# Kernel optimization log

Measured on AMD Instinct MI355X. Metric: run time of the kernel, lower is better.

Reference implementation:

```python
import jax, jax.numpy as jnp
import numpy as np

B, S, HID = 2, 2048, 2048
NH, NKV = 32, 8
HD = HID // NH          # 64
G = NH // NKV           # 4 query heads per kv head
ROPE_BASE = 10000.0


def _rope_cos_sin(seq_len, head_dim, dtype):
    inv_freq = 1.0 / (ROPE_BASE ** (jnp.arange(0, head_dim, 2, dtype=jnp.float32) / head_dim))
    freqs = jnp.arange(seq_len, dtype=jnp.float32)[:, None] * inv_freq[None, :]  # [S, HD/2]
    cos = jnp.cos(freqs)
    sin = jnp.sin(freqs)
    # torch code does cos.repeat(1, 2): tile along last dim -> [S, HD]
    cos = jnp.concatenate([cos, cos], axis=-1).astype(dtype)
    sin = jnp.concatenate([sin, sin], axis=-1).astype(dtype)
    return cos, sin


def _rotate_half(x):
    x1, x2 = jnp.split(x, 2, axis=-1)
    return jnp.concatenate([-x2, x1], axis=-1)


def setup_inputs() -> dict:
    key = jax.random.key(0)
    ks = jax.random.split(key, 5)
    sc = 0.02
    return {
        "hidden_states": jax.random.normal(ks[0], (B, S, HID), dtype=jnp.float32),
        "wq": jax.random.normal(ks[1], (HID, HID), dtype=jnp.float32) * sc,
        "wk": jax.random.normal(ks[2], (NKV * HD, HID), dtype=jnp.float32) * sc,
        "wv": jax.random.normal(ks[3], (NKV * HD, HID), dtype=jnp.float32) * sc,
        "wo": jax.random.normal(ks[4], (HID, HID), dtype=jnp.float32) * sc,
    }


def reference(hidden_states, wq, wk, wv, wo):
    b, s, _ = hidden_states.shape
    # projections (torch Linear: y = x @ W^T)
    q = (hidden_states @ wq.T).reshape(b, s, NH, HD).transpose(0, 2, 1, 3)   # [B,NH,S,HD]
    k = (hidden_states @ wk.T).reshape(b, s, NKV, HD).transpose(0, 2, 1, 3)  # [B,NKV,S,HD]
    v = (hidden_states @ wv.T).reshape(b, s, NKV, HD).transpose(0, 2, 1, 3)  # [B,NKV,S,HD]

    cos, sin = _rope_cos_sin(s, HD, q.dtype)  # [S,HD]
    q = q * cos + _rotate_half(q) * sin
    k = k * cos + _rotate_half(k) * sin

    # GQA: group query heads per kv head instead of repeat_interleave (same math)
    qg = q.reshape(b, NKV, G, s, HD)
    scale = HD ** -0.5
    scores = jnp.einsum('bkgsd,bktd->bkgst', qg, k) * scale     # [B,NKV,G,S,S]
    attn = jax.nn.softmax(scores, axis=-1)
    out = jnp.einsum('bkgst,bktd->bkgsd', attn, v)              # [B,NKV,G,S,HD]
    out = out.reshape(b, NH, s, HD).transpose(0, 2, 1, 3).reshape(b, s, HID)
    return out @ wo.T
```

## Files before the change

### kernel.cpp

```cpp
#include <hip/hip_runtime.h>
#include <stdint.h>

typedef __attribute__((ext_vector_type(8))) short bf16x8;
typedef __attribute__((ext_vector_type(4))) short bf16x4;
typedef __attribute__((ext_vector_type(4))) float f32x4;
typedef __attribute__((ext_vector_type(4))) unsigned u32x4;
typedef __attribute__((ext_vector_type(2))) unsigned u32x2;

#define S_LEN 2048
#define HIDDEN 2048
#define N_HEADS 32
#define N_KV 8
#define HEAD_DIM 64
#define KVD (N_KV * HEAD_DIM)

__device__ __forceinline__ float bf2f(short u) {
  return __builtin_bit_cast(float, ((unsigned)(unsigned short)u) << 16);
}
__device__ __forceinline__ short f2bf(float f) {
  unsigned u = __builtin_bit_cast(unsigned, f);
  u += 0x7FFFu + ((u >> 16) & 1u);
  return (short)(u >> 16);
}
__device__ __forceinline__ unsigned cvtpk(float lo, float hi) {
  unsigned r;
  asm("v_cvt_pk_bf16_f32 %0, %1, %2" : "=v"(r) : "v"(lo), "v"(hi));
  return r;
}
__device__ __forceinline__ bf16x8 cvt8(f32x4 lo, f32x4 hi) {
  bf16x8 r;
#pragma unroll
  for (int j = 0; j < 4; ++j) { r[j] = f2bf(lo[j]); r[j + 4] = f2bf(hi[j]); }
  return r;
}
__device__ __forceinline__ void storeC(float* p, float v) { *p = v; }
__device__ __forceinline__ void storeC(short* p, float v) { *p = f2bf(v); }

__device__ __forceinline__ void gll16(const void* g, void* l) {
  __builtin_amdgcn_global_load_lds(
      (const __attribute__((address_space(1))) void*)g,
      (__attribute__((address_space(3))) void*)l, 16, 0, 0);
}

struct CvtArgs {
  const float* src[5];
  short* dst[5];
  int cnt4[5];
};
__global__ void cvt_bf16(CvtArgs a, int total4) {
  int u = blockIdx.x * 256 + threadIdx.x;
  const int stride = gridDim.x * 256;
  for (; u < total4; u += stride) {
    int s = 0, off = u;
    while (off >= a.cnt4[s]) { off -= a.cnt4[s]; ++s; }
    f32x4 v = *(const f32x4*)(a.src[s] + (size_t)off * 4);
    bf16x4 r;
#pragma unroll
    for (int j = 0; j < 4; ++j) r[j] = f2bf(v[j]);
    *(bf16x4*)(a.dst[s] + (size_t)off * 4) = r;
  }
}

template <typename CT>
__launch_bounds__(256, 3)
__global__ void gemm_lds(const short* __restrict__ A, const short* __restrict__ W,
                         CT* __restrict__ C, int M, int N, int K) {
  __shared__ short As[128 * 32];
  __shared__ short Ws[128 * 32];
  const int tid  = threadIdx.x;
  const int lane = tid & 63;
  const int w    = tid >> 6;
  const int wm = w >> 1, wn = w & 1;
  const int lr = lane & 15, lg = lane >> 4;
  const int m0 = blockIdx.y * 128, n0 = blockIdx.x * 128;

  const size_t a0 = (size_t)(m0 + w * 16 + (lane >> 2)) * K + (lane & 3) * 8;
  const size_t a1 = a0 + (size_t)64 * K;
  const size_t b0 = (size_t)(n0 + w * 16 + (lane >> 2)) * K + (lane & 3) * 8;
  const size_t b1 = b0 + (size_t)64 * K;
  short* lA0 = &As[(w * 16) * 32];
  short* lA1 = &As[(64 + w * 16) * 32];
  short* lB0 = &Ws[(w * 16) * 32];
  short* lB1 = &Ws[(64 + w * 16) * 32];

  f32x4 acc[4][4] = {};

  for (int k0 = 0; k0 < K; k0 += 32) {
    __syncthreads();
    gll16(A + a0 + k0, lA0);
    gll16(A + a1 + k0, lA1);
    gll16(W + b0 + k0, lB0);
    gll16(W + b1 + k0, lB1);
    __syncthreads();
    bf16x8 af[4], bfr[4];
#pragma unroll
    for (int i = 0; i < 4; ++i) {
      af[i]  = *(const bf16x8*)&As[(wm * 64 + i * 16 + lr) * 32 + lg * 8];
      bfr[i] = *(const bf16x8*)&Ws[(wn * 64 + i * 16 + lr) * 32 + lg * 8];
    }
#pragma unroll
    for (int i = 0; i < 4; ++i)
#pragma unroll
      for (int j = 0; j < 4; ++j)
        acc[i][j] = __builtin_amdgcn_mfma_f32_16x16x32_bf16(af[i], bfr[j], acc[i][j], 0, 0, 0);
  }

#pragma unroll
  for (int i = 0; i < 4; ++i)
#pragma unroll
    for (int j = 0; j < 4; ++j) {
      const int row = m0 + wm * 64 + i * 16 + lg * 4;
      const int col = n0 + wn * 64 + j * 16 + lr;
#pragma unroll
      for (int r = 0; r < 4; ++r)
        storeC(&C[(size_t)(row + r) * N + col], acc[i][j][r]);
    }
}

template <typename AT, typename CT>
__launch_bounds__(256, 2)
__global__ void gemm_bt(const AT* __restrict__ A, const float* __restrict__ W,
                        CT* __restrict__ C, int M, int N, int K) {
  __shared__ short As[128][40];
  __shared__ short Ws[128][40];
  const int tid  = threadIdx.x;
  const int lane = tid & 63;
  const int wid  = tid >> 6;
  const int wm = wid >> 1, wn = wid & 1;
  const int lr = lane & 15, lg = lane >> 4;
  const int m0 = blockIdx.y * 128, n0 = blockIdx.x * 128;
  const int srow = tid >> 2;
  const int scol = (tid & 3) * 8;

  f32x4 acc[4][4] = {};
  const AT*    Ap = A + (size_t)(m0 + srow) * K + scol;
  const float* Wp = W + (size_t)(n0 + srow) * K + scol;

  for (int k0 = 0; k0 < K; k0 += 32) {
    bf16x8 a0, a1, b0, b1;
    if constexpr (sizeof(AT) == 4) {
      a0 = cvt8(*(const f32x4*)(Ap + k0), *(const f32x4*)(Ap + k0 + 4));
      a1 = cvt8(*(const f32x4*)(Ap + (size_t)64 * K + k0),
                *(const f32x4*)(Ap + (size_t)64 * K + k0 + 4));
    } else {
      a0 = *(const bf16x8*)(Ap + k0);
      a1 = *(const bf16x8*)(Ap + (size_t)64 * K + k0);
    }
    b0 = cvt8(*(const f32x4*)(Wp + k0), *(const f32x4*)(Wp + k0 + 4));
    b1 = cvt8(*(const f32x4*)(Wp + (size_t)64 * K + k0),
              *(const f32x4*)(Wp + (size_t)64 * K + k0 + 4));
    __syncthreads();
    *(bf16x8*)&As[srow][scol]      = a0;
    *(bf16x8*)&As[srow + 64][scol] = a1;
    *(bf16x8*)&Ws[srow][scol]      = b0;
    *(bf16x8*)&Ws[srow + 64][scol] = b1;
    __syncthreads();
    bf16x8 af[4], bfr[4];
#pragma unroll
    for (int i = 0; i < 4; ++i) {
      af[i]  = *(const bf16x8*)&As[wm * 64 + i * 16 + lr][lg * 8];
      bfr[i] = *(const bf16x8*)&Ws[wn * 64 + i * 16 + lr][lg * 8];
    }
#pragma unroll
    for (int i = 0; i < 4; ++i)
#pragma unroll
      for (int j = 0; j < 4; ++j)
        acc[i][j] = __builtin_amdgcn_mfma_f32_16x16x32_bf16(af[i], bfr[j], acc[i][j], 0, 0, 0);
  }
#pragma unroll
  for (int i = 0; i < 4; ++i)
#pragma unroll
    for (int j = 0; j < 4; ++j) {
      const int row = m0 + wm * 64 + i * 16 + lg * 4;
      const int col = n0 + wn * 64 + j * 16 + lr;
#pragma unroll
      for (int r = 0; r < 4; ++r)
        storeC(&C[(size_t)(row + r) * N + col], acc[i][j][r]);
    }
}

template <int NH>
__global__ void rope_kernel(short* __restrict__ buf, int rowstride, int total) {
  int idx = blockIdx.x * 256 + threadIdx.x;
  if (idx >= total) return;
  const int i   = idx & 31;
  const int hh  = (idx >> 5) % NH;
  const int row = (idx >> 5) / NH;
  const int pos = row & (S_LEN - 1);
  const float invf = exp2f(-(float)i * (13.287712379549449f / 32.0f));
  const float ang  = (float)pos * invf;
  float sn, c;
  sincosf(ang, &sn, &c);
  size_t base = (size_t)row * rowstride + hh * 64;
  float x1 = bf2f(buf[base + i]);
  float x2 = bf2f(buf[base + i + 32]);
  buf[base + i]      = f2bf(x1 * c - x2 * sn);
  buf[base + i + 32] = f2bf(x2 * c + x1 * sn);
}

#define NT (S_LEN / 64)
__launch_bounds__(256, 2)
__global__ void attn_kernel(const short* __restrict__ Q, const short* __restrict__ K,
                            const short* __restrict__ V, short* __restrict__ O,
                            int qs, int ks_, int os) {
  const int qt = blockIdx.x, h = blockIdx.y, b = blockIdx.z;
  const int kv = h >> 2;
  const int tid  = threadIdx.x;
  const int lane = tid & 63, w = tid >> 6;
  const int lr = lane & 15, lg = lane >> 4;

  __shared__ short Vt[2][64][72];

  const int q0 = qt * 128 + w * 32;
  bf16x8 qa[2][2];
#pragma unroll
  for (int fr = 0; fr < 2; ++fr) {
    const short* qp = Q + (size_t)(b * S_LEN + q0 + fr * 16 + lr) * qs + h * HEAD_DIM + lg * 8;
    qa[fr][0] = *(const bf16x8*)qp;
    qa[fr][1] = *(const bf16x8*)(qp + 32);
  }

  f32x4 o[2][4] = {};
  float mrow[2] = {-1e30f, -1e30f};
  float msc[2]  = {-1e30f, -1e30f};
  float lsum[2] = {0.f, 0.f};

  const int vdb   = w * 16;
  const int cperm = (lane & 32) + ((lane >> 2) & 3) * 8 + ((lane >> 4) & 1) * 4 + (lane & 3);
  const short* vbase = V + ((size_t)(b * S_LEN) + lane) * ks_ + kv * HEAD_DIM + vdb;
  bf16x8 vp0 = *(const bf16x8*)vbase;
  bf16x8 vp1 = *(const bf16x8*)(vbase + 8);

  const short* kbase = K + (size_t)(b * S_LEN + lr) * ks_ + kv * HEAD_DIM + lg * 8;
  bf16x8 kf[4][2];
#pragma unroll
  for (int nf = 0; nf < 4; ++nf) {
    kf[nf][0] = *(const bf16x8*)(kbase + (size_t)nf * 16 * ks_);
    kf[nf][1] = *(const bf16x8*)(kbase + (size_t)nf * 16 * ks_ + 32);
  }

  const float SC   = 0.125f * 1.4426950408889634f;
  const float THRR = 8.0f / SC;

  for (int kt = 0; kt < NT; ++kt) {
    const int cur = kt & 1;
#pragma unroll
    for (int j = 0; j < 8; ++j) Vt[cur][vdb + j][cperm] = vp0[j];
#pragma unroll
    for (int j = 0; j < 8; ++j) Vt[cur][vdb + 8 + j][cperm] = vp1[j];
    __syncthreads();
    if (kt + 1 < NT) {
      const short* vp = vbase + (size_t)(kt + 1) * 64 * ks_;
      vp0 = *(const bf16x8*)vp;
      vp1 = *(const bf16x8*)(vp + 8);
    }
    f32x4 sf[2][4];
    __builtin_amdgcn_s_setprio(1);
#pragma unroll
    for (int nf = 0; nf < 4; ++nf)
#pragma unroll
      for (int fr = 0; fr < 2; ++fr) {
        f32x4 t = {};
        t = __builtin_amdgcn_mfma_f32_16x16x32_bf16(kf[nf][0], qa[fr][0], t, 0, 0, 0);
        t = __builtin_amdgcn_mfma_f32_16x16x32_bf16(kf[nf][1], qa[fr][1], t, 0, 0, 0);
        sf[fr][nf] = t;
      }
    __builtin_amdgcn_s_setprio(0);
    if (kt + 1 < NT) {
      const short* kp = kbase + (size_t)(kt + 1) * 64 * ks_;
#pragma unroll
      for (int nf = 0; nf < 4; ++nf) {
        kf[nf][0] = *(const bf16x8*)(kp + (size_t)nf * 16 * ks_);
        kf[nf][1] = *(const bf16x8*)(kp + (size_t)nf * 16 * ks_ + 32);
      }
    }
    bf16x8 pa[2][2];
#pragma unroll
    for (int fr = 0; fr < 2; ++fr) {
      float lmax = fmaxf(fmaxf(sf[fr][0][0], sf[fr][0][1]), fmaxf(sf[fr][0][2], sf[fr][0][3]));
#pragma unroll
      for (int nf = 1; nf < 4; ++nf) {
        float m01 = fmaxf(sf[fr][nf][0], sf[fr][nf][1]);
        float m23 = fmaxf(sf[fr][nf][2], sf[fr][nf][3]);
        lmax = fmaxf(lmax, fmaxf(m01, m23));
      }
      if (!__all(lmax <= mrow[fr] + THRR)) {
        float mx = fmaxf(lmax, __shfl_xor(lmax, 16));
        mx = fmaxf(mx, __shfl_xor(mx, 32));
        const float mnew  = fmaxf(mrow[fr], mx);
        const float alpha = exp2f((mrow[fr] - mnew) * SC);
        mrow[fr] = mnew;
        msc[fr]  = mnew * SC;
        lsum[fr] *= alpha;
#pragma unroll
        for (int df = 0; df < 4; ++df) o[fr][df] *= alpha;
      }
      const float nm = msc[fr];
      float s = 0.f;
#pragma unroll
      for (int nf = 0; nf < 4; ++nf)
#pragma unroll
        for (int r = 0; r < 4; ++r) {
          float pv = exp2f(fmaf(sf[fr][nf][r], SC, -nm));
          sf[fr][nf][r] = pv;
          s += pv;
        }
      lsum[fr] += s;
#pragma unroll
      for (int ks2 = 0; ks2 < 2; ++ks2) {
        u32x4 pk;
        pk[0] = cvtpk(sf[fr][2 * ks2][0], sf[fr][2 * ks2][1]);
        pk[1] = cvtpk(sf[fr][2 * ks2][2], sf[fr][2 * ks2][3]);
        pk[2] = cvtpk(sf[fr][2 * ks2 + 1][0], sf[fr][2 * ks2 + 1][1]);
        pk[3] = cvtpk(sf[fr][2 * ks2 + 1][2], sf[fr][2 * ks2 + 1][3]);
        pa[fr][ks2] = __builtin_bit_cast(bf16x8, pk);
      }
    }
    __builtin_amdgcn_s_setprio(1);
#pragma unroll
    for (int ks2 = 0; ks2 < 2; ++ks2) {
      bf16x8 vb[4];
#pragma unroll
      for (int df = 0; df < 4; ++df)
        vb[df] = *(const bf16x8*)&Vt[cur][df * 16 + lr][ks2 * 32 + lg * 8];
#pragma unroll
      for (int fr = 0; fr < 2; ++fr)
#pragma unroll
        for (int df = 0; df < 4; ++df)
          o[fr][df] = __builtin_amdgcn_mfma_f32_16x16x32_bf16(vb[df], pa[fr][ks2], o[fr][df], 0, 0, 0);
    }
    __builtin_amdgcn_s_setprio(0);
  }

#pragma unroll
  for (int fr = 0; fr < 2; ++fr) {
    float ls = lsum[fr];
    ls += __shfl_xor(ls, 16);
    ls += __shfl_xor(ls, 32);
    const float invl = 1.0f / ls;
    const size_t orow = (size_t)(b * S_LEN + q0 + fr * 16 + lr) * os + h * HEAD_DIM;
#pragma unroll
    for (int df = 0; df < 4; ++df) {
      u32x2 pk;
      pk[0] = cvtpk(o[fr][df][0] * invl, o[fr][df][1] * invl);
      pk[1] = cvtpk(o[fr][df][2] * invl, o[fr][df][3] * invl);
      *(u32x2*)&O[orow + df * 16 + 4 * lg] = pk;
    }
  }
}

extern "C" void kernel_launch(void* const* d_in, const int* in_sizes, int n_in,
                              void* d_out, int out_size, void* d_ws, size_t ws_size,
                              hipStream_t stream) {
  (void)in_sizes; (void)n_in; (void)out_size;
  const float* hidden = (const float*)d_in[0];
  const float* wq = (const float*)d_in[1];
  const float* wk = (const float*)d_in[2];
  const float* wv = (const float*)d_in[3];
  const float* wo = (const float*)d_in[4];
  float* out = (float*)d_out;

  const int M = 2 * S_LEN;
  const size_t nHid  = (size_t)M * HIDDEN;
  const size_t nW    = (size_t)HIDDEN * HIDDEN;
  const size_t nWkv  = (size_t)KVD * HIDDEN;
  const size_t nWcat = nW + 2 * nWkv;
  const int    NQKV  = HIDDEN + 2 * KVD;
  const size_t nQKV  = (size_t)M * NQKV;

  const size_t fastElems = nHid + nWcat + nW + nQKV + nHid;
  if (ws_size >= fastElems * sizeof(short)) {
    short* hb   = (short*)d_ws;
    short* wcat = hb + nHid;
    short* wob  = wcat + nWcat;
    short* QKV  = wob + nW;
    short* AO   = QKV + nQKV;

    CvtArgs ca;
    ca.src[0] = hidden; ca.dst[0] = hb;            ca.cnt4[0] = (int)(nHid / 4);
    ca.src[1] = wq;     ca.dst[1] = wcat;          ca.cnt4[1] = (int)(nW / 4);
    ca.src[2] = wk;     ca.dst[2] = wcat + nW;     ca.cnt4[2] = (int)(nWkv / 4);
    ca.src[3] = wv;     ca.dst[3] = wcat + nW + nWkv; ca.cnt4[3] = (int)(nWkv / 4);
    ca.src[4] = wo;     ca.dst[4] = wob;           ca.cnt4[4] = (int)(nW / 4);
    const int total4 = (int)((nHid + nWcat + nW) / 4);
    cvt_bf16<<<2048, 256, 0, stream>>>(ca, total4);

    gemm_lds<short><<<dim3(NQKV / 128, 32), 256, 0, stream>>>(hb, wcat, QKV, M, NQKV, HIDDEN);
    const int rtot = M * 40 * 32;
    rope_kernel<40><<<(rtot + 255) / 256, 256, 0, stream>>>(QKV, NQKV, rtot);
    attn_kernel<<<dim3(S_LEN / 128, N_HEADS, 2), 256, 0, stream>>>(
        QKV, QKV + HIDDEN, QKV + HIDDEN + KVD, AO, NQKV, NQKV, HIDDEN);
    gemm_lds<float><<<dim3(16, 32), 256, 0, stream>>>(AO, wob, out, M, HIDDEN, HIDDEN);
  } else {
    short* Qb = (short*)d_ws;
    short* Kb = Qb + nHid;
    short* Vb = Kb + (size_t)M * KVD;
    short* AO = Vb + (size_t)M * KVD;
    gemm_bt<float, short><<<dim3(16, 32), 256, 0, stream>>>(hidden, wq, Qb, M, HIDDEN, HIDDEN);
    gemm_bt<float, short><<<dim3(4, 32), 256, 0, stream>>>(hidden, wk, Kb, M, KVD, HIDDEN);
    gemm_bt<float, short><<<dim3(4, 32), 256, 0, stream>>>(hidden, wv, Vb, M, KVD, HIDDEN);
    const int rq = M * N_HEADS * 32, rk = M * N_KV * 32;
    rope_kernel<N_HEADS><<<(rq + 255) / 256, 256, 0, stream>>>(Qb, HIDDEN, rq);
    rope_kernel<N_KV><<<(rk + 255) / 256, 256, 0, stream>>>(Kb, KVD, rk);
    attn_kernel<<<dim3(S_LEN / 128, N_HEADS, 2), 256, 0, stream>>>(
        Qb, Kb, Vb, AO, HIDDEN, KVD, HIDDEN);
    gemm_bt<short, float><<<dim3(16, 32), 256, 0, stream>>>(AO, wo, out, M, HIDDEN, HIDDEN);
  }
}
```

Measured before the change: 294.9 us.

## Software-pipeline QK^T one tile ahead of softmax/PV and swizzle GEMM block order

The attention loop is unrolled by two and computes QK^T scores for the next KV tile before doing softmax and PV on the current tile, using ping-pong score buffers. This lets MFMA work overlap with the exp/max VALU work. The GEMM kernel also remaps block IDs in groups of 8 so that neighbouring workgroups land differently across XCDs and get better L2 locality. The extra score registers may raise register pressure and could reduce occupancy.

```diff
diff --git a/kernel.cpp b/kernel.cpp
--- a/kernel.cpp
+++ b/kernel.cpp
@@ -72,7 +72,18 @@
   const int w    = tid >> 6;
   const int wm = w >> 1, wn = w & 1;
   const int lr = lane & 15, lg = lane >> 4;
-  const int m0 = blockIdx.y * 128, n0 = blockIdx.x * 128;
+
+  int bx = blockIdx.x, by = blockIdx.y;
+  {
+    const int nwg = gridDim.x * gridDim.y;
+    if ((nwg & 7) == 0) {
+      const int bid = by * gridDim.x + bx;
+      const int id2 = (bid & 7) * (nwg >> 3) + (bid >> 3);
+      bx = id2 % gridDim.x;
+      by = id2 / gridDim.x;
+    }
+  }
+  const int m0 = by * 128, n0 = bx * 128;
 
   const size_t a0 = (size_t)(m0 + w * 16 + (lane >> 2)) * K + (lane & 3) * 8;
   const size_t a1 = a0 + (size_t)64 * K;
@@ -198,6 +209,94 @@
   buf[base + i + 32] = f2bf(x2 * c + x1 * sn);
 }
 
+__device__ __forceinline__ void qkt_mfma(const bf16x8 (&kf)[4][2],
+                                         const bf16x8 (&qa)[2][2],
+                                         f32x4 (&sf)[2][4]) {
+  __builtin_amdgcn_s_setprio(1);
+#pragma unroll
+  for (int nf = 0; nf < 4; ++nf)
+#pragma unroll
+    for (int fr = 0; fr < 2; ++fr) {
+      f32x4 t = {};
+      t = __builtin_amdgcn_mfma_f32_16x16x32_bf16(kf[nf][0], qa[fr][0], t, 0, 0, 0);
+      t = __builtin_amdgcn_mfma_f32_16x16x32_bf16(kf[nf][1], qa[fr][1], t, 0, 0, 0);
+      sf[fr][nf] = t;
+    }
+  __builtin_amdgcn_s_setprio(0);
+}
+
+__device__ __forceinline__ void load_kf(bf16x8 (&kf)[4][2], const short* kbase,
+                                        int t, int ks_) {
+  const short* kp = kbase + (size_t)t * 64 * ks_;
+#pragma unroll
+  for (int nf = 0; nf < 4; ++nf) {
+    kf[nf][0] = *(const bf16x8*)(kp + (size_t)nf * 16 * ks_);
+    kf[nf][1] = *(const bf16x8*)(kp + (size_t)nf * 16 * ks_ + 32);
+  }
+}
+
+__device__ __forceinline__ void softmax_pv(
+    f32x4 (&sf)[2][4], const short (*vt)[72], f32x4 (&o)[2][4],
+    float (&mrow)[2], float (&msc)[2], float (&lsum)[2],
+    int lr, int lg, float SC, float THRR) {
+  bf16x8 pa[2][2];
+#pragma unroll
+  for (int fr = 0; fr < 2; ++fr) {
+    float lmax = fmaxf(fmaxf(sf[fr][0][0], sf[fr][0][1]), fmaxf(sf[fr][0][2], sf[fr][0][3]));
+#pragma unroll
+    for (int nf = 1; nf < 4; ++nf) {
+      float m01 = fmaxf(sf[fr][nf][0], sf[fr][nf][1]);
+      float m23 = fmaxf(sf[fr][nf][2], sf[fr][nf][3]);
+      lmax = fmaxf(lmax, fmaxf(m01, m23));
+    }
+    if (!__all(lmax <= mrow[fr] + THRR)) {
+      float mx = fmaxf(lmax, __shfl_xor(lmax, 16));
+      mx = fmaxf(mx, __shfl_xor(mx, 32));
+      const float mnew  = fmaxf(mrow[fr], mx);
+      const float alpha = exp2f((mrow[fr] - mnew) * SC);
+      mrow[fr] = mnew;
+      msc[fr]  = mnew * SC;
+      lsum[fr] *= alpha;
+#pragma unroll
+      for (int df = 0; df < 4; ++df) o[fr][df] *= alpha;
+    }
+    const float nm = msc[fr];
+    float s = 0.f;
+#pragma unroll
+    for (int nf = 0; nf < 4; ++nf)
+#pragma unroll
+      for (int r = 0; r < 4; ++r) {
+        float pv = exp2f(fmaf(sf[fr][nf][r], SC, -nm));
+        sf[fr][nf][r] = pv;
+        s += pv;
+      }
+    lsum[fr] += s;
+#pragma unroll
+    for (int ks2 = 0; ks2 < 2; ++ks2) {
+      u32x4 pk;
+      pk[0] = cvtpk(sf[fr][2 * ks2][0], sf[fr][2 * ks2][1]);
+      pk[1] = cvtpk(sf[fr][2 * ks2][2], sf[fr][2 * ks2][3]);
+      pk[2] = cvtpk(sf[fr][2 * ks2 + 1][0], sf[fr][2 * ks2 + 1][1]);
+      pk[3] = cvtpk(sf[fr][2 * ks2 + 1][2], sf[fr][2 * ks2 + 1][3]);
+      pa[fr][ks2] = __builtin_bit_cast(bf16x8, pk);
+    }
+  }
+  __builtin_amdgcn_s_setprio(1);
+#pragma unroll
+  for (int ks2 = 0; ks2 < 2; ++ks2) {
+    bf16x8 vb[4];
+#pragma unroll
+    for (int df = 0; df < 4; ++df)
+      vb[df] = *(const bf16x8*)&vt[df * 16 + lr][ks2 * 32 + lg * 8];
+#pragma unroll
+    for (int fr = 0; fr < 2; ++fr)
+#pragma unroll
+      for (int df = 0; df < 4; ++df)
+        o[fr][df] = __builtin_amdgcn_mfma_f32_16x16x32_bf16(vb[df], pa[fr][ks2], o[fr][df], 0, 0, 0);
+  }
+  __builtin_amdgcn_s_setprio(0);
+}
+
 #define NT (S_LEN / 64)
 __launch_bounds__(256, 2)
 __global__ void attn_kernel(const short* __restrict__ Q, const short* __restrict__ K,
@@ -228,108 +327,47 @@
   const int vdb   = w * 16;
   const int cperm = (lane & 32) + ((lane >> 2) & 3) * 8 + ((lane >> 4) & 1) * 4 + (lane & 3);
   const short* vbase = V + ((size_t)(b * S_LEN) + lane) * ks_ + kv * HEAD_DIM + vdb;
+  const short* kbase = K + (size_t)(b * S_LEN + lr) * ks_ + kv * HEAD_DIM + lg * 8;
+
+  const float SC   = 0.125f * 1.4426950408889634f;
+  const float THRR = 8.0f / SC;
+
   bf16x8 vp0 = *(const bf16x8*)vbase;
   bf16x8 vp1 = *(const bf16x8*)(vbase + 8);
-
-  const short* kbase = K + (size_t)(b * S_LEN + lr) * ks_ + kv * HEAD_DIM + lg * 8;
   bf16x8 kf[4][2];
-#pragma unroll
-  for (int nf = 0; nf < 4; ++nf) {
-    kf[nf][0] = *(const bf16x8*)(kbase + (size_t)nf * 16 * ks_);
-    kf[nf][1] = *(const bf16x8*)(kbase + (size_t)nf * 16 * ks_ + 32);
-  }
-
-  const float SC   = 0.125f * 1.4426950408889634f;
-  const float THRR = 8.0f / SC;
-
-  for (int kt = 0; kt < NT; ++kt) {
-    const int cur = kt & 1;
-#pragma unroll
-    for (int j = 0; j < 8; ++j) Vt[cur][vdb + j][cperm] = vp0[j];
-#pragma unroll
-    for (int j = 0; j < 8; ++j) Vt[cur][vdb + 8 + j][cperm] = vp1[j];
-    __syncthreads();
-    if (kt + 1 < NT) {
-      const short* vp = vbase + (size_t)(kt + 1) * 64 * ks_;
+  f32x4 sfA[2][4], sfB[2][4];
+  load_kf(kf, kbase, 0, ks_);
+  qkt_mfma(kf, qa, sfA);
+  load_kf(kf, kbase, 1, ks_);
+
+  for (int t = 0; t < NT; t += 2) {
+#pragma unroll
+    for (int j = 0; j < 8; ++j) Vt[0][vdb + j][cperm] = vp0[j];
+#pragma unroll
+    for (int j = 0; j < 8; ++j) Vt[0][vdb + 8 + j][cperm] = vp1[j];
+    __syncthreads();
+    {
+      const short* vp = vbase + (size_t)(t + 1) * 64 * ks_;
       vp0 = *(const bf16x8*)vp;
       vp1 = *(const bf16x8*)(vp + 8);
     }
-    f32x4 sf[2][4];
-    __builtin_amdgcn_s_setprio(1);
-#pragma unroll
-    for (int nf = 0; nf < 4; ++nf)
-#pragma unroll
-      for (int fr = 0; fr < 2; ++fr) {
-        f32x4 t = {};
-        t = __builtin_amdgcn_mfma_f32_16x16x32_bf16(kf[nf][0], qa[fr][0], t, 0, 0, 0);
-        t = __builtin_amdgcn_mfma_f32_16x16x32_bf16(kf[nf][1], qa[fr][1], t, 0, 0, 0);
-        sf[fr][nf] = t;
-      }
-    __builtin_amdgcn_s_setprio(0);
-    if (kt + 1 < NT) {
-      const short* kp = kbase + (size_t)(kt + 1) * 64 * ks_;
-#pragma unroll
-      for (int nf = 0; nf < 4; ++nf) {
-        kf[nf][0] = *(const bf16x8*)(kp + (size_t)nf * 16 * ks_);
-        kf[nf][1] = *(const bf16x8*)(kp + (size_t)nf * 16 * ks_ + 32);
-      }
-    }
-    bf16x8 pa[2][2];
-#pragma unroll
-    for (int fr = 0; fr < 2; ++fr) {
-      float lmax = fmaxf(fmaxf(sf[fr][0][0], sf[fr][0][1]), fmaxf(sf[fr][0][2], sf[fr][0][3]));
-#pragma unroll
-      for (int nf = 1; nf < 4; ++nf) {
-        float m01 = fmaxf(sf[fr][nf][0], sf[fr][nf][1]);
-        float m23 = fmaxf(sf[fr][nf][2], sf[fr][nf][3]);
-        lmax = fmaxf(lmax, fmaxf(m01, m23));
-      }
-      if (!__all(lmax <= mrow[fr] + THRR)) {
-        float mx = fmaxf(lmax, __shfl_xor(lmax, 16));
-        mx = fmaxf(mx, __shfl_xor(mx, 32));
-        const float mnew  = fmaxf(mrow[fr], mx);
-        const float alpha = exp2f((mrow[fr] - mnew) * SC);
-        mrow[fr] = mnew;
-        msc[fr]  = mnew * SC;
-        lsum[fr] *= alpha;
-#pragma unroll
-        for (int df = 0; df < 4; ++df) o[fr][df] *= alpha;
-      }
-      const float nm = msc[fr];
-      float s = 0.f;
-#pragma unroll
-      for (int nf = 0; nf < 4; ++nf)
-#pragma unroll
-        for (int r = 0; r < 4; ++r) {
-          float pv = exp2f(fmaf(sf[fr][nf][r], SC, -nm));
-          sf[fr][nf][r] = pv;
-          s += pv;
-        }
-      lsum[fr] += s;
-#pragma unroll
-      for (int ks2 = 0; ks2 < 2; ++ks2) {
-        u32x4 pk;
-        pk[0] = cvtpk(sf[fr][2 * ks2][0], sf[fr][2 * ks2][1]);
-        pk[1] = cvtpk(sf[fr][2 * ks2][2], sf[fr][2 * ks2][3]);
-        pk[2] = cvtpk(sf[fr][2 * ks2 + 1][0], sf[fr][2 * ks2 + 1][1]);
-        pk[3] = cvtpk(sf[fr][2 * ks2 + 1][2], sf[fr][2 * ks2 + 1][3]);
-        pa[fr][ks2] = __builtin_bit_cast(bf16x8, pk);
-      }
-    }
-    __builtin_amdgcn_s_setprio(1);
-#pragma unroll
-    for (int ks2 = 0; ks2 < 2; ++ks2) {
-      bf16x8 vb[4];
-#pragma unroll
-      for (int df = 0; df < 4; ++df)
-        vb[df] = *(const bf16x8*)&Vt[cur][df * 16 + lr][ks2 * 32 + lg * 8];
-#pragma unroll
-      for (int fr = 0; fr < 2; ++fr)
-#pragma unroll
-        for (int df = 0; df < 4; ++df)
-          o[fr][df] = __builtin_amdgcn_mfma_f32_16x16x32_bf16(vb[df], pa[fr][ks2], o[fr][df], 0, 0, 0);
-    }
-    __builtin_amdgcn_s_setprio(0);
+    qkt_mfma(kf, qa, sfB);
+    if (t + 2 < NT) load_kf(kf, kbase, t + 2, ks_);
+    softmax_pv(sfA, Vt[0], o, mrow, msc, lsum, lr, lg, SC, THRR);
+
+#pragma unroll
+    for (int j = 0; j < 8; ++j) Vt[1][vdb + j][cperm] = vp0[j];
+#pragma unroll
+    for (int j = 0; j < 8; ++j) Vt[1][vdb + 8 + j][cperm] = vp1[j];
+    __syncthreads();
+    if (t + 2 < NT) {
+      const short* vp = vbase + (size_t)(t + 2) * 64 * ks_;
+      vp0 = *(const bf16x8*)vp;
+      vp1 = *(const bf16x8*)(vp + 8);
+      qkt_mfma(kf, qa, sfA);
+    }
+    if (t + 3 < NT) load_kf(kf, kbase, t + 3, ks_);
+    softmax_pv(sfB, Vt[1], o, mrow, msc, lsum, lr, lg, SC, THRR);
   }
 
 #pragma unroll
```

New measurement: 293.0 us. No clear change (-0.6%).
